# Optimization experiments

Hardware: AMD Instinct MI355X
Metric: run time of the kernel (lower is better)

## Reference

```python
import jax, jax.numpy as jnp
import numpy as np
import math

N_EMBD = 1024
BLOCK_SIZE = 2048
B = 4

def setup_inputs() -> dict:
    key = jax.random.key(0)
    ks = jax.random.split(key, 9)
    s = 0.02
    return {
        "q": jax.random.normal(ks[0], (B, BLOCK_SIZE, N_EMBD), jnp.float32),
        "k": jax.random.normal(ks[1], (B, BLOCK_SIZE, N_EMBD), jnp.float32),
        "v": jax.random.normal(ks[2], (B, BLOCK_SIZE, N_EMBD), jnp.float32),
        "wq_w": jax.random.normal(ks[3], (N_EMBD, N_EMBD), jnp.float32) * s,
        "wq_b": jax.random.normal(ks[4], (N_EMBD,), jnp.float32) * s,
        "wk_w": jax.random.normal(ks[5], (N_EMBD, N_EMBD), jnp.float32) * s,
        "wk_b": jax.random.normal(ks[6], (N_EMBD,), jnp.float32) * s,
        "wv_w": jax.random.normal(ks[7], (N_EMBD, N_EMBD), jnp.float32) * s,
        "wv_b": jax.random.normal(ks[8], (N_EMBD,), jnp.float32) * s,
        "causal": 1,
    }

def reference(q, k, v, wq_w, wq_b, wk_w, wk_b, wv_w, wv_b, causal):
    # torch Linear: y = x @ W.T + b
    qp = jnp.einsum('bte,oe->bto', q, wq_w) + wq_b
    kp = jnp.einsum('bte,oe->bto', k, wk_w) + wk_b
    vp = jnp.einsum('bte,oe->bto', v, wv_w) + wv_b
    scale = 1.0 / math.sqrt(N_EMBD)
    weights = jnp.einsum('bqe,bke->bqk', qp, kp) * scale  # [B,T1,T2]
    if causal:
        T1, T2 = qp.shape[1], kp.shape[1]
        mask = jnp.tril(jnp.ones((T1, T2), dtype=bool))
        weights = jnp.where(mask, weights, -jnp.inf)
    attn = jax.nn.softmax(weights, axis=-1)
    return jnp.einsum('bqk,bke->bqe', attn, vp)
```

## Files before the change

kernel.cpp:

```cpp
#include <hip/hip_runtime.h>
#include <hip/hip_bf16.h>
#include <cstdint>
#include <math.h>

#define T 2048
#define NE 1024
#define NB 4

typedef __attribute__((ext_vector_type(8))) short short8;
typedef __attribute__((ext_vector_type(4))) short shortx4;
typedef __attribute__((ext_vector_type(4))) float floatx4;

__device__ __forceinline__ unsigned short f2bf(float f) {
    unsigned u = __float_as_uint(f);
    u += 0x7FFF + ((u >> 16) & 1);
    return (unsigned short)(u >> 16);
}

__device__ __forceinline__ shortx4 cvt4(floatx4 f) {
    __hip_bfloat162 a = __float22bfloat162_rn(float2{f[0], f[1]});
    __hip_bfloat162 b = __float22bfloat162_rn(float2{f[2], f[3]});
    union { shortx4 s; unsigned u[2]; } r;
    r.u[0] = *(unsigned*)&a; r.u[1] = *(unsigned*)&b;
    return r.s;
}

__device__ __forceinline__ void gl2lds(const void* g, void* l) {
    __builtin_amdgcn_global_load_lds(
        (const __attribute__((address_space(1))) void*)g,
        (__attribute__((address_space(3))) void*)l, 16, 0, 0);
}

template<int NWROW, int BIAS_MODE, bool OUT_F32, bool CKLIM, bool DUAL, int MODE>
__global__ __launch_bounds__(NWROW * 128, 4) void gemm_bf16(
    const unsigned short* __restrict__ A0, const unsigned short* __restrict__ A1,
    const unsigned short* __restrict__ B0, const unsigned short* __restrict__ B1,
    const float* __restrict__ bias0, const float* __restrict__ bias1,
    void* __restrict__ C0, void* __restrict__ C1,
    int K, int lda, int ldb, int ldc,
    size_t sA, size_t sB, size_t sC, float scale, int ntnShift)
{
    constexpr int NTHR = NWROW * 128;
    int tm, tn;
    const int bz = blockIdx.z;
    if (MODE == 2) {
        const int i = blockIdx.x;
        int lin = (i & 7) * 17 + (i >> 3);
        tm = (int)((sqrtf(8.f * (float)lin + 1.f) - 1.f) * 0.5f);
        while ((tm + 1) * (tm + 2) / 2 <= lin) ++tm;
        while (tm * (tm + 1) / 2 > lin) --tm;
        tn = lin - tm * (tm + 1) / 2;
    } else if (MODE == 1) {
        const int bid = blockIdx.x;
        const int lin = (bid & 7) * (gridDim.x >> 3) + (bid >> 3);
        tm = lin >> ntnShift; tn = lin & ((1 << ntnShift) - 1);
    } else if (MODE == 3) {
        const int xcd = blockIdx.x & 7, j = blockIdx.x >> 3;
        tm = (j & 1) ? xcd : (15 - xcd);
        tn = j >> 1;
    } else {
        tn = blockIdx.x; tm = blockIdx.y;
    }

    __shared__ __align__(16) char As[NWROW * 64 * 128];
    __shared__ __align__(16) char Bs[128 * 128];

    const int tid = threadIdx.x, lane = tid & 63, wave = tid >> 6;
    const int wm = wave % NWROW, wn = wave / NWROW;
    const int quad = lane >> 4, l15 = lane & 15;
    const int p = l15 & 7;
    const int r8 = lane >> 3, c8 = lane & 7;

    const char* Ab = (const char*)((DUAL && bz) ? A1 : A0) + (size_t)bz * sA * 2;
    const char* Bb = (const char*)((DUAL && bz) ? B1 : B0) + (size_t)bz * sB * 2;
    const float* bias = (DUAL && bz) ? bias1 : bias0;

    int Keff = K;
    if (CKLIM) { int kl = (tm + 1) * 128; Keff = kl < K ? kl : K; }

    const size_t ldab = (size_t)lda * 2, ldbb = (size_t)ldb * 2;
    const char* gA = Ab + (size_t)(tm * (NWROW * 64) + wave * 8 + r8) * ldab + (size_t)((c8 ^ r8) * 16);
    const char* gB = Bb + (size_t)(tn * 128 + wave * 8 + r8) * ldbb + (size_t)((c8 ^ r8) * 16);
    char* lA = As + wave * 1024;
    char* lB = Bs + wave * 1024;
    constexpr int BCALLS = 8 / NWROW;

    floatx4 acc[4][4] = {};

    for (int k0 = 0; k0 < Keff; k0 += 64) {
        const size_t kb = (size_t)k0 * 2;
        #pragma unroll
        for (int c = 0; c < 4; ++c)
            gl2lds(gA + (size_t)(c * NWROW * 16) * ldab + kb, lA + c * NTHR * 16);
        #pragma unroll
        for (int c = 0; c < BCALLS; ++c)
            gl2lds(gB + (size_t)(c * NWROW * 16) * ldbb + kb, lB + c * NTHR * 16);
        __syncthreads();

        #pragma unroll
        for (int kk = 0; kk < 2; kk++) {
            short8 af[4], bfr[4];
            #pragma unroll
            for (int i = 0; i < 4; i++)
                af[i] = *(const short8*)(As + (wm * 64 + i * 16 + l15) * 128 + (((kk * 4 + quad) ^ p) << 4));
            #pragma unroll
            for (int j = 0; j < 4; j++)
                bfr[j] = *(const short8*)(Bs + (wn * 64 + j * 16 + l15) * 128 + (((kk * 4 + quad) ^ p) << 4));
            #pragma unroll
            for (int i = 0; i < 4; i++)
                #pragma unroll
                for (int j = 0; j < 4; j++)
                    acc[i][j] = __builtin_amdgcn_mfma_f32_16x16x32_bf16(af[i], bfr[j], acc[i][j], 0, 0, 0);
        }
        __syncthreads();
    }

    char* Cb = (char*)((DUAL && bz) ? C1 : C0) + (size_t)bz * sC * (OUT_F32 ? 4 : 2);
    #pragma unroll
    for (int i = 0; i < 4; i++) {
        #pragma unroll
        for (int j = 0; j < 4; j++) {
            const int n = tn * 128 + wn * 64 + j * 16 + l15;
            #pragma unroll
            for (int r = 0; r < 4; r++) {
                const int m = tm * (NWROW * 64) + wm * 64 + i * 16 + quad * 4 + r;
                float val = acc[i][j][r] * scale;
                if (BIAS_MODE == 1) val += bias[n];
                if (BIAS_MODE == 2) val += bias[m];
                if (OUT_F32) ((float*)Cb)[(size_t)m * ldc + n] = val;
                else         ((unsigned short*)Cb)[(size_t)m * ldc + n] = f2bf(val);
            }
        }
    }
}

__global__ __launch_bounds__(256, 4) void fused12(
    const unsigned short* __restrict__ qb, const unsigned short* __restrict__ kb,
    const unsigned short* __restrict__ vb,
    const unsigned short* __restrict__ wqb, const unsigned short* __restrict__ wkb,
    const unsigned short* __restrict__ wvb,
    const float* __restrict__ wq_b, const float* __restrict__ wk_b,
    const float* __restrict__ wv_b,
    unsigned short* __restrict__ qp, unsigned short* __restrict__ kp,
    unsigned short* __restrict__ vpT)
{
    const int bid = blockIdx.x;
    const unsigned short *A, *B; const float* bias; unsigned short* C;
    int tm, tn, ldc, biasN;
    if (bid < 1024) {
        const int z = bid >> 9, l0 = bid & 511;
        const int lin = (l0 & 7) * 64 + (l0 >> 3);
        tm = lin >> 3; tn = lin & 7;
        A = z ? kb : qb; B = z ? wkb : wqb; bias = z ? wk_b : wq_b; C = z ? kp : qp;
        ldc = NE; biasN = 1;
    } else {
        const int t = bid - 1024, z = t >> 7, l0 = t & 127;
        const int lin = (l0 & 7) * 16 + (l0 >> 3);
        tm = lin >> 4; tn = lin & 15;
        A = wvb; B = vb + (size_t)z * T * NE; bias = wv_b; C = vpT + (size_t)z * NE * T;
        ldc = T; biasN = 0;
    }

    __shared__ __align__(16) char As[128 * 128];
    __shared__ __align__(16) char Bs[128 * 128];

    const int tid = threadIdx.x, lane = tid & 63, wave = tid >> 6;
    const int wm = wave & 1, wn = wave >> 1;
    const int quad = lane >> 4, l15 = lane & 15;
    const int p = l15 & 7;
    const int r8 = lane >> 3, c8 = lane & 7;

    const size_t ldab = (size_t)NE * 2;
    const char* gA = (const char*)A + (size_t)(tm * 128 + wave * 8 + r8) * ldab + (size_t)((c8 ^ r8) * 16);
    const char* gB = (const char*)B + (size_t)(tn * 128 + wave * 8 + r8) * ldab + (size_t)((c8 ^ r8) * 16);
    char* lA = As + wave * 1024;
    char* lB = Bs + wave * 1024;

    floatx4 acc[4][4] = {};

    for (int k0 = 0; k0 < NE; k0 += 64) {
        const size_t kb2 = (size_t)k0 * 2;
        #pragma unroll
        for (int c = 0; c < 4; ++c)
            gl2lds(gA + (size_t)(c * 32) * ldab + kb2, lA + c * 4096);
        #pragma unroll
        for (int c = 0; c < 4; ++c)
            gl2lds(gB + (size_t)(c * 32) * ldab + kb2, lB + c * 4096);
        __syncthreads();

        #pragma unroll
        for (int kk = 0; kk < 2; kk++) {
            short8 af[4], bfr[4];
            #pragma unroll
            for (int i = 0; i < 4; i++)
                af[i] = *(const short8*)(As + (wm * 64 + i * 16 + l15) * 128 + (((kk * 4 + quad) ^ p) << 4));
            #pragma unroll
            for (int j = 0; j < 4; j++)
                bfr[j] = *(const short8*)(Bs + (wn * 64 + j * 16 + l15) * 128 + (((kk * 4 + quad) ^ p) << 4));
            #pragma unroll
            for (int i = 0; i < 4; i++)
                #pragma unroll
                for (int j = 0; j < 4; j++)
                    acc[i][j] = __builtin_amdgcn_mfma_f32_16x16x32_bf16(af[i], bfr[j], acc[i][j], 0, 0, 0);
        }
        __syncthreads();
    }

    #pragma unroll
    for (int i = 0; i < 4; i++) {
        #pragma unroll
        for (int j = 0; j < 4; j++) {
            const int n = tn * 128 + wn * 64 + j * 16 + l15;
            #pragma unroll
            for (int r = 0; r < 4; r++) {
                const int m = tm * 128 + wm * 64 + i * 16 + quad * 4 + r;
                float val = acc[i][j][r] + (biasN ? bias[n] : bias[m]);
                C[(size_t)m * ldc + n] = f2bf(val);
            }
        }
    }
}

__global__ __launch_bounds__(256) void cvt_all(
    const float* __restrict__ q, const float* __restrict__ k, const float* __restrict__ v,
    const float* __restrict__ wq, const float* __restrict__ wk, const float* __restrict__ wv,
    unsigned short* __restrict__ qb, unsigned short* __restrict__ kb, unsigned short* __restrict__ vb,
    unsigned short* __restrict__ wqb, unsigned short* __restrict__ wkb, unsigned short* __restrict__ wvb)
{
    const int IN4 = NB * T * NE / 4;
    const int W4  = NE * NE / 4;
    int i = blockIdx.x * 256 + threadIdx.x;
    const float* s; unsigned short* d; int j;
    if (i < 3 * IN4) {
        int sel = i >> 21; j = i & (IN4 - 1);
        s = sel == 0 ? q : sel == 1 ? k : v;
        d = sel == 0 ? qb : sel == 1 ? kb : vb;
    } else {
        int t2 = i - 3 * IN4; int sel = t2 >> 18; j = t2 & (W4 - 1);
        s = sel == 0 ? wq : sel == 1 ? wk : wv;
        d = sel == 0 ? wqb : sel == 1 ? wkb : wvb;
    }
    floatx4 f = ((const floatx4*)s)[j];
    ((shortx4*)d)[j] = cvt4(f);
}

__global__ __launch_bounds__(256) void softmax_causal(unsigned short* __restrict__ S)
{
    const int row = blockIdx.x;
    const int b = row >> 11, r = row & 2047;
    unsigned short* p = S + ((size_t)b * T + (size_t)r) * T;
    const int nv = r + 1;
    const int lim = ((r >> 7) + 1) * 128;
    const int tid = threadIdx.x, lane = tid & 63, wave = tid >> 6;
    const int c0 = tid * 8;
    const bool act = c0 < lim;

    short8 raw = {};
    if (act) raw = ((const short8*)p)[tid];
    float x[8];
    float mx = -3.0e38f;
    #pragma unroll
    for (int j = 0; j < 8; j++) {
        float vv = -3.0e38f;
        if (c0 + j < nv) vv = __uint_as_float((unsigned)(unsigned short)raw[j] << 16);
        x[j] = vv;
        mx = fmaxf(mx, vv);
    }
    #pragma unroll
    for (int off = 32; off > 0; off >>= 1)
        mx = fmaxf(mx, __shfl_xor(mx, off));
    __shared__ float smax[4], ssum[4];
    if (lane == 0) smax[wave] = mx;
    __syncthreads();
    mx = fmaxf(fmaxf(smax[0], smax[1]), fmaxf(smax[2], smax[3]));

    float s = 0.f;
    #pragma unroll
    for (int j = 0; j < 8; j++) {
        float e = 0.f;
        if (c0 + j < nv) e = __expf(x[j] - mx);
        x[j] = e;
        s += e;
    }
    #pragma unroll
    for (int off = 32; off > 0; off >>= 1)
        s += __shfl_xor(s, off);
    if (lane == 0) ssum[wave] = s;
    __syncthreads();
    const float inv = 1.f / (ssum[0] + ssum[1] + ssum[2] + ssum[3]);

    if (act) {
        short8 o;
        #pragma unroll
        for (int j = 0; j < 8; j++)
            o[j] = (short)f2bf(x[j] * inv);
        ((short8*)p)[tid] = o;
    }
}

extern "C" void kernel_launch(void* const* d_in, const int* in_sizes, int n_in,
                              void* d_out, int out_size, void* d_ws, size_t ws_size,
                              hipStream_t stream)
{
    const float* q    = (const float*)d_in[0];
    const float* k    = (const float*)d_in[1];
    const float* v    = (const float*)d_in[2];
    const float* wq_w = (const float*)d_in[3];
    const float* wq_b = (const float*)d_in[4];
    const float* wk_w = (const float*)d_in[5];
    const float* wk_b = (const float*)d_in[6];
    const float* wv_w = (const float*)d_in[7];
    const float* wv_b = (const float*)d_in[8];

    const size_t INEL = (size_t)NB * T * NE;

    unsigned short* qp = (unsigned short*)d_out;
    unsigned short* kp = qp + INEL;

    unsigned short* vpT = (unsigned short*)d_ws;
    unsigned short* S   = vpT + (size_t)NB * NE * T;
    unsigned short* qb  = S;
    unsigned short* kb  = qb + INEL;
    unsigned short* vb  = kb + INEL;
    unsigned short* wqb = vb + INEL;
    unsigned short* wkb = wqb + (size_t)NE * NE;
    unsigned short* wvb = wkb + (size_t)NE * NE;

    dim3 blk(256);

    const int NCVT = (3 * (int)(INEL / 4) + 3 * NE * NE / 4 + 255) / 256;
    cvt_all<<<dim3(NCVT), blk, 0, stream>>>(q, k, v, wq_w, wk_w, wv_w, qb, kb, vb, wqb, wkb, wvb);

    fused12<<<dim3(1536), blk, 0, stream>>>(
        qb, kb, vb, wqb, wkb, wvb, wq_b, wk_b, wv_b, qp, kp, vpT);

    gemm_bf16<2, 0, false, false, false, 2><<<dim3(136, 1, NB), blk, 0, stream>>>(
        qp, nullptr, kp, nullptr, nullptr, nullptr, S, nullptr,
        NE, NE, NE, T, (size_t)T * NE, (size_t)T * NE, (size_t)T * T, 0.03125f, 0);

    softmax_causal<<<dim3(NB * T), blk, 0, stream>>>(S);

    gemm_bf16<2, 0, true, true, false, 3><<<dim3(128, 1, NB), blk, 0, stream>>>(
        S, nullptr, vpT, nullptr, nullptr, nullptr, d_out, nullptr,
        T, T, T, NE, (size_t)T * T, (size_t)NE * T, (size_t)T * NE, 1.0f, 0);
}
```

Before: 292.1 us.

## Fuse causal softmax into QK and PV GEMM epilogues with atomic row sums

Removes the standalone softmax kernel. The QK^T GEMM epilogue now writes unnormalized exp(score) with causal masking and atomically accumulates per-row sums into a workspace buffer zeroed by a memset. The PV GEMM epilogue scales each output row by the reciprocal of its row sum. This avoids a full read/write pass over the score matrix, at the cost of dropping max-subtraction, which risks overflow for large-magnitude scores, and adding atomic contention.

```diff
diff --git a/kernel.cpp b/kernel.cpp
--- a/kernel.cpp
+++ b/kernel.cpp
@@ -31,7 +31,7 @@
         (__attribute__((address_space(3))) void*)l, 16, 0, 0);
 }
 
-template<int NWROW, int BIAS_MODE, bool OUT_F32, bool CKLIM, bool DUAL, int MODE>
+template<int NWROW, int BIAS_MODE, bool OUT_F32, bool CKLIM, bool DUAL, int MODE, int EPI>
 __global__ __launch_bounds__(NWROW * 128, 4) void gemm_bf16(
     const unsigned short* __restrict__ A0, const unsigned short* __restrict__ A1,
     const unsigned short* __restrict__ B0, const unsigned short* __restrict__ B1,
@@ -116,6 +116,45 @@
     }
 
     char* Cb = (char*)((DUAL && bz) ? C1 : C0) + (size_t)bz * sC * (OUT_F32 ? 4 : 2);
+
+    if constexpr (EPI == 1) {
+        float* rs = (float*)C1 + (size_t)bz * T;
+        #pragma unroll
+        for (int i = 0; i < 4; i++) {
+            #pragma unroll
+            for (int r = 0; r < 4; r++) {
+                const int m = tm * (NWROW * 64) + wm * 64 + i * 16 + quad * 4 + r;
+                float rsum = 0.f;
+                #pragma unroll
+                for (int j = 0; j < 4; j++) {
+                    const int n = tn * 128 + wn * 64 + j * 16 + l15;
+                    float e = 0.f;
+                    if (n <= m) e = __expf(acc[i][j][r] * scale);
+                    rsum += e;
+                    ((unsigned short*)Cb)[(size_t)m * ldc + n] = f2bf(e);
+                }
+                rsum += __shfl_xor(rsum, 1);
+                rsum += __shfl_xor(rsum, 2);
+                rsum += __shfl_xor(rsum, 4);
+                rsum += __shfl_xor(rsum, 8);
+                if (l15 == 0) atomicAdd(&rs[m], rsum);
+            }
+        }
+        return;
+    }
+
+    float inv[4][4];
+    if constexpr (EPI == 2) {
+        const float* rsp = bias0 + (size_t)bz * T;
+        #pragma unroll
+        for (int i = 0; i < 4; i++)
+            #pragma unroll
+            for (int r = 0; r < 4; r++) {
+                const int m = tm * (NWROW * 64) + wm * 64 + i * 16 + quad * 4 + r;
+                inv[i][r] = 1.0f / rsp[m];
+            }
+    }
+
     #pragma unroll
     for (int i = 0; i < 4; i++) {
         #pragma unroll
@@ -127,6 +166,7 @@
                 float val = acc[i][j][r] * scale;
                 if (BIAS_MODE == 1) val += bias[n];
                 if (BIAS_MODE == 2) val += bias[m];
+                if (EPI == 2) val *= inv[i][r];
                 if (OUT_F32) ((float*)Cb)[(size_t)m * ldc + n] = val;
                 else         ((unsigned short*)Cb)[(size_t)m * ldc + n] = f2bf(val);
             }
@@ -244,60 +284,6 @@
     ((shortx4*)d)[j] = cvt4(f);
 }
 
-__global__ __launch_bounds__(256) void softmax_causal(unsigned short* __restrict__ S)
-{
-    const int row = blockIdx.x;
-    const int b = row >> 11, r = row & 2047;
-    unsigned short* p = S + ((size_t)b * T + (size_t)r) * T;
-    const int nv = r + 1;
-    const int lim = ((r >> 7) + 1) * 128;
-    const int tid = threadIdx.x, lane = tid & 63, wave = tid >> 6;
-    const int c0 = tid * 8;
-    const bool act = c0 < lim;
-
-    short8 raw = {};
-    if (act) raw = ((const short8*)p)[tid];
-    float x[8];
-    float mx = -3.0e38f;
-    #pragma unroll
-    for (int j = 0; j < 8; j++) {
-        float vv = -3.0e38f;
-        if (c0 + j < nv) vv = __uint_as_float((unsigned)(unsigned short)raw[j] << 16);
-        x[j] = vv;
-        mx = fmaxf(mx, vv);
-    }
-    #pragma unroll
-    for (int off = 32; off > 0; off >>= 1)
-        mx = fmaxf(mx, __shfl_xor(mx, off));
-    __shared__ float smax[4], ssum[4];
-    if (lane == 0) smax[wave] = mx;
-    __syncthreads();
-    mx = fmaxf(fmaxf(smax[0], smax[1]), fmaxf(smax[2], smax[3]));
-
-    float s = 0.f;
-    #pragma unroll
-    for (int j = 0; j < 8; j++) {
-        float e = 0.f;
-        if (c0 + j < nv) e = __expf(x[j] - mx);
-        x[j] = e;
-        s += e;
-    }
-    #pragma unroll
-    for (int off = 32; off > 0; off >>= 1)
-        s += __shfl_xor(s, off);
-    if (lane == 0) ssum[wave] = s;
-    __syncthreads();
-    const float inv = 1.f / (ssum[0] + ssum[1] + ssum[2] + ssum[3]);
-
-    if (act) {
-        short8 o;
-        #pragma unroll
-        for (int j = 0; j < 8; j++)
-            o[j] = (short)f2bf(x[j] * inv);
-        ((short8*)p)[tid] = o;
-    }
-}
-
 extern "C" void kernel_launch(void* const* d_in, const int* in_sizes, int n_in,
                               void* d_out, int out_size, void* d_ws, size_t ws_size,
                               hipStream_t stream)
@@ -325,6 +311,7 @@
     unsigned short* wqb = vb + INEL;
     unsigned short* wkb = wqb + (size_t)NE * NE;
     unsigned short* wvb = wkb + (size_t)NE * NE;
+    float* rowsum = (float*)((char*)d_ws + 52ull * 1024 * 1024);
 
     dim3 blk(256);
 
@@ -334,13 +321,13 @@
     fused12<<<dim3(1536), blk, 0, stream>>>(
         qb, kb, vb, wqb, wkb, wvb, wq_b, wk_b, wv_b, qp, kp, vpT);
 
-    gemm_bf16<2, 0, false, false, false, 2><<<dim3(136, 1, NB), blk, 0, stream>>>(
-        qp, nullptr, kp, nullptr, nullptr, nullptr, S, nullptr,
+    hipMemsetAsync(rowsum, 0, (size_t)NB * T * sizeof(float), stream);
+
+    gemm_bf16<2, 0, false, false, false, 2, 1><<<dim3(136, 1, NB), blk, 0, stream>>>(
+        qp, nullptr, kp, nullptr, nullptr, nullptr, S, rowsum,
         NE, NE, NE, T, (size_t)T * NE, (size_t)T * NE, (size_t)T * T, 0.03125f, 0);
 
-    softmax_causal<<<dim3(NB * T), blk, 0, stream>>>(S);
-
-    gemm_bf16<2, 0, true, true, false, 3><<<dim3(128, 1, NB), blk, 0, stream>>>(
-        S, nullptr, vpT, nullptr, nullptr, nullptr, d_out, nullptr,
+    gemm_bf16<2, 0, true, true, false, 3, 2><<<dim3(128, 1, NB), blk, 0, stream>>>(
+        S, nullptr, vpT, nullptr, rowsum, nullptr, d_out, nullptr,
         T, T, T, NE, (size_t)T * T, (size_t)NE * T, (size_t)T * NE, 1.0f, 0);
 }
```

Result: faster. 286.2 us (-2.0%).
